# Kernel optimization log

Hardware: AMD Instinct MI355X
Metric: run time of the kernel (lower is better)

## Reference

```python
import jax, jax.numpy as jnp
import numpy as np

BUCKET_SIZE = 256
LOOK_BACKWARD = 1
LOOK_FORWARD = 0  # causal


def look_around(x, backward, forward, pad_value):
    # x: (b, n_buckets, w, ...) -> (b, n_buckets, w*(backward+forward+1), ...)
    n = x.shape[1]
    pads = [(0, 0)] * x.ndim
    pads[1] = (backward, forward)
    p = jnp.pad(x, pads, constant_values=pad_value)
    return jnp.concatenate([p[:, i:i + n] for i in range(backward + forward + 1)], axis=2)


def setup_inputs() -> dict:
    key = jax.random.key(0)
    kq, kk, kv = jax.random.split(key, 3)
    shape = (2, 16, 4096, 64)  # [batch, heads, seq, head_dim]
    q = jax.random.normal(kq, shape, dtype=jnp.float32)
    k = jax.random.normal(kk, shape, dtype=jnp.float32)
    v = jax.random.normal(kv, shape, dtype=jnp.float32)
    return {"q": q, "k": k, "v": v}


def reference(q, k, v):
    shape = q.shape
    t, e = shape[-2], shape[-1]
    merge = lambda x: x.reshape(-1, t, e)
    q, k, v = merge(q), merge(k), merge(v)
    b = q.shape[0]
    buckets = t // BUCKET_SIZE

    bucket_fn = lambda x: x.reshape(b, buckets, BUCKET_SIZE, e)
    bq, bk, bv = bucket_fn(q), bucket_fn(k), bucket_fn(v)

    bk = look_around(bk, LOOK_BACKWARD, LOOK_FORWARD, 0.0)
    bv = look_around(bv, LOOK_BACKWARD, LOOK_FORWARD, 0.0)

    ticker = jnp.arange(t, dtype=jnp.int32).reshape(1, buckets, BUCKET_SIZE)
    bq_t = ticker  # (1, buckets, w)
    bq_k = look_around(ticker, LOOK_BACKWARD, LOOK_FORWARD, -1)  # (1, buckets, w*(lb+lf+1))

    dots = jnp.einsum('bnie,bnje->bnij', bq, bk) * (e ** -0.5)
    mask_value = -jnp.finfo(dots.dtype).max

    causal_mask = bq_t[:, :, :, None] < bq_k[:, :, None, :]
    pad_mask = (bq_k == -1)[:, :, None, :]
    dots = jnp.where(causal_mask | pad_mask, mask_value, dots)

    attn = jax.nn.softmax(dots, axis=-1)
    out = jnp.einsum('bnij,bnje->bnie', attn, bv)
    return out.reshape(shape)
```

## Files before the change

kernel.cpp:

```cpp
#include <hip/hip_runtime.h>

typedef __bf16 bf16x8 __attribute__((ext_vector_type(8)));
typedef float f32x16 __attribute__((ext_vector_type(16)));
typedef int i32x2 __attribute__((ext_vector_type(2)));
typedef unsigned int u32;

static __device__ __forceinline__ u32 cvt_pk_bf16(float lo, float hi) {
    u32 r;
    asm("v_cvt_pk_bf16_f32 %0, %1, %2" : "=v"(r) : "v"(lo), "v"(hi));
    return r;
}

__global__ __launch_bounds__(256, 1)
void local_attn_kernel(const float* __restrict__ qg, const float* __restrict__ kg,
                       const float* __restrict__ vg, float* __restrict__ og)
{
    __shared__ __align__(16) __bf16 sK[2][64][64];
    __shared__ __align__(16) u32 sVp[2][64][32];

    const int bid = ((blockIdx.x & 7) << 7) | (blockIdx.x >> 3);
    const int bh = bid >> 5, bi = (bid >> 1) & 15, qh = bid & 1;
    const int tid = threadIdx.x, w = tid >> 6;
    const int lane = tid & 63, l31 = lane & 31, h = lane >> 5;

    const long long base = (long long)bh << 18;
    const float* qp = qg + base + ((long long)bi << 14);
    const float* kp = kg + base + (((long long)(bi - 1)) << 14);
    const float* vp = vg + base + (((long long)(bi - 1)) << 14);
    float*       op = og + base + ((long long)bi << 14);

    const int qb0 = qh * 128 + w * 32;

    bf16x8 qf[4];
    {
        const float QS = 0.18033688011112042f;
        const float* qrow = qp + (qb0 + l31) * 64 + 8 * h;
#pragma unroll
        for (int ks = 0; ks < 4; ++ks) {
            float4 f0 = *(const float4*)(qrow + ks * 16);
            float4 f1 = *(const float4*)(qrow + ks * 16 + 4);
            bf16x8 t;
            t[0] = (__bf16)(f0.x * QS); t[1] = (__bf16)(f0.y * QS);
            t[2] = (__bf16)(f0.z * QS); t[3] = (__bf16)(f0.w * QS);
            t[4] = (__bf16)(f1.x * QS); t[5] = (__bf16)(f1.y * QS);
            t[6] = (__bf16)(f1.z * QS); t[7] = (__bf16)(f1.w * QS);
            qf[ks] = t;
        }
    }

    f32x16 o0, o1;
#pragma unroll
    for (int i = 0; i < 16; ++i) { o0[i] = 0.f; o1[i] = 0.f; }
    float lsum = 0.f;

    const int skey = tid >> 3, stg = tid & 7;
    const int kslot = (stg ^ (skey & 7)) << 3;
    const int vkp = tid >> 4, vd0 = (tid & 15) * 4;
    const int vkq0 = vkp >> 2, vkq1 = vkq0 + 4, vj = vkp & 3;
    const int x0 = ((vd0 + 0) & 7) ^ (((vd0 + 0) >> 2) & 7);
    const int x1 = ((vd0 + 1) & 7) ^ (((vd0 + 1) >> 2) & 7);
    const int x2 = ((vd0 + 2) & 7) ^ (((vd0 + 2) >> 2) & 7);
    const int x3 = ((vd0 + 3) & 7) ^ (((vd0 + 3) >> 2) & 7);
    const float* kA = kp + skey * 64 + stg * 8;
    const float* vA = vp + (2 * vkp) * 64 + vd0;

    const int c0 = (bi == 0) ? 4 : 0;
    const int NCHB = 6 + 2 * qh;
    const int qpos = qb0 + l31;
    const int wlim = qb0 + 287;

    int cur = 0;
    float4 k0r, k1r, k2r, k3r, v0r, v1r, v2r, v3r;

#define STAGE_LOAD(c) do {                                   \
        const float* ks_ = kA + (c) * (64 * 64);             \
        k0r = *(const float4*)ks_;                           \
        k1r = *(const float4*)(ks_ + 4);                     \
        k2r = *(const float4*)(ks_ + 2048);                  \
        k3r = *(const float4*)(ks_ + 2052);                  \
        const float* vs_ = vA + (c) * (64 * 64);             \
        v0r = *(const float4*)vs_;                           \
        v1r = *(const float4*)(vs_ + 64);                    \
        v2r = *(const float4*)(vs_ + 2048);                  \
        v3r = *(const float4*)(vs_ + 2112);                  \
    } while (0)

#define STAGE_WRITE(buf) do {                                                     \
        union { u32 u[4]; bf16x8 b; } kva_, kvb_;                                 \
        kva_.u[0] = cvt_pk_bf16(k0r.x, k0r.y);                                    \
        kva_.u[1] = cvt_pk_bf16(k0r.z, k0r.w);                                    \
        kva_.u[2] = cvt_pk_bf16(k1r.x, k1r.y);                                    \
        kva_.u[3] = cvt_pk_bf16(k1r.z, k1r.w);                                    \
        *(bf16x8*)&sK[buf][skey][kslot] = kva_.b;                                 \
        kvb_.u[0] = cvt_pk_bf16(k2r.x, k2r.y);                                    \
        kvb_.u[1] = cvt_pk_bf16(k2r.z, k2r.w);                                    \
        kvb_.u[2] = cvt_pk_bf16(k3r.x, k3r.y);                                    \
        kvb_.u[3] = cvt_pk_bf16(k3r.z, k3r.w);                                    \
        *(bf16x8*)&sK[buf][skey + 32][kslot] = kvb_.b;                            \
        sVp[buf][vd0 + 0][((vkq0 ^ x0) << 2) + vj] = cvt_pk_bf16(v0r.x, v1r.x);   \
        sVp[buf][vd0 + 1][((vkq0 ^ x1) << 2) + vj] = cvt_pk_bf16(v0r.y, v1r.y);   \
        sVp[buf][vd0 + 2][((vkq0 ^ x2) << 2) + vj] = cvt_pk_bf16(v0r.z, v1r.z);   \
        sVp[buf][vd0 + 3][((vkq0 ^ x3) << 2) + vj] = cvt_pk_bf16(v0r.w, v1r.w);   \
        sVp[buf][vd0 + 0][((vkq1 ^ x0) << 2) + vj] = cvt_pk_bf16(v2r.x, v3r.x);   \
        sVp[buf][vd0 + 1][((vkq1 ^ x1) << 2) + vj] = cvt_pk_bf16(v2r.y, v3r.y);   \
        sVp[buf][vd0 + 2][((vkq1 ^ x2) << 2) + vj] = cvt_pk_bf16(v2r.z, v3r.z);   \
        sVp[buf][vd0 + 3][((vkq1 ^ x3) << 2) + vj] = cvt_pk_bf16(v2r.w, v3r.w);   \
    } while (0)

    STAGE_LOAD(c0);
    STAGE_WRITE(0);

    for (int c = c0; c < NCHB; ++c) {
        __syncthreads();
        const bool pf = (c + 1 < NCHB);
        if (pf) STAGE_LOAD(c + 1);

        const int kbase = c * 64;
#pragma unroll
        for (int kt = 0; kt < 2; ++kt) {
            const int kb0 = kbase + 32 * kt;
            if (kb0 > wlim) continue;

            const int key = kt * 32 + l31;
            const int ksw = key & 7;
            bf16x8 kfa[4];
#pragma unroll
            for (int ks = 0; ks < 4; ++ks)
                kfa[ks] = *(const bf16x8*)&sK[cur][key][((ks * 2 + h) ^ ksw) << 3];
            f32x16 s;
#pragma unroll
            for (int i2 = 0; i2 < 16; ++i2) s[i2] = 0.f;
#pragma unroll
            for (int ks = 0; ks < 4; ++ks)
                s = __builtin_amdgcn_mfma_f32_32x32x16_bf16(kfa[ks], qf[ks], s, 0, 0, 0);

            u32 wds[8];
            if (kb0 + 31 <= qb0 + 256) {
#pragma unroll
                for (int m = 0; m < 8; ++m) {
                    const float e0 = __builtin_amdgcn_exp2f(s[2 * m]);
                    const float e1 = __builtin_amdgcn_exp2f(s[2 * m + 1]);
                    lsum += e0 + e1;
                    wds[m] = cvt_pk_bf16(e0, e1);
                }
            } else {
                const int jb = kb0 + 4 * h;
#pragma unroll
                for (int m = 0; m < 8; ++m) {
                    const int r0 = 2 * m, r1 = 2 * m + 1;
                    const int j0 = jb + (r0 & 3) + 8 * (r0 >> 2);
                    const int j1 = jb + (r1 & 3) + 8 * (r1 >> 2);
                    float e0 = __builtin_amdgcn_exp2f(s[r0]);
                    float e1 = __builtin_amdgcn_exp2f(s[r1]);
                    e0 = (j0 > qpos + 256) ? 0.f : e0;
                    e1 = (j1 > qpos + 256) ? 0.f : e1;
                    lsum += e0 + e1;
                    wds[m] = cvt_pk_bf16(e0, e1);
                }
            }

#pragma unroll
            for (int kis = 0; kis < 2; ++kis) {
                i32x2 r02 = __builtin_amdgcn_permlane32_swap(
                    (int)wds[4 * kis + 0], (int)wds[4 * kis + 2], false, false);
                i32x2 r13 = __builtin_amdgcn_permlane32_swap(
                    (int)wds[4 * kis + 1], (int)wds[4 * kis + 3], false, false);
                union { u32 u[4]; bf16x8 b; } pu;
                pu.u[0] = (u32)r02.x; pu.u[1] = (u32)r13.x;
                pu.u[2] = (u32)r02.y; pu.u[3] = (u32)r13.y;

                const int G = (kt * 2 + kis) * 2 + h;
                const int sl = G ^ (l31 & 7) ^ ((l31 >> 2) & 7);
                bf16x8 vb0 = *(const bf16x8*)&sVp[cur][l31][sl << 2];
                bf16x8 vb1 = *(const bf16x8*)&sVp[cur][32 + l31][sl << 2];
                o0 = __builtin_amdgcn_mfma_f32_32x32x16_bf16(pu.b, vb0, o0, 0, 0, 0);
                o1 = __builtin_amdgcn_mfma_f32_32x32x16_bf16(pu.b, vb1, o1, 0, 0, 0);
            }
        }

        if (pf) STAGE_WRITE(cur ^ 1);
        cur ^= 1;
    }

    lsum += __shfl_xor(lsum, 32, 64);
    const float inv = 1.0f / lsum;
#pragma unroll
    for (int r = 0; r < 16; ++r) {
        const int qr = (r & 3) + 8 * (r >> 2) + 4 * h;
        const float iq = __shfl(inv, qr, 64);
        float* orow = op + (qb0 + qr) * 64;
        orow[l31]      = o0[r] * iq;
        orow[32 + l31] = o1[r] * iq;
    }
}

extern "C" void kernel_launch(void* const* d_in, const int* in_sizes, int n_in,
                              void* d_out, int out_size, void* d_ws, size_t ws_size,
                              hipStream_t stream) {
    const float* q = (const float*)d_in[0];
    const float* k = (const float*)d_in[1];
    const float* v = (const float*)d_in[2];
    float* out = (float*)d_out;
    local_attn_kernel<<<dim3(1024), dim3(256), 0, stream>>>(q, k, v, out);
}
```

Measured before the change: 42.07 us.

## Use one 512-thread block per bucket and load K directly from global

Merges the two query-half blocks into a single 512-thread block covering all 256 queries of a bucket, so the shared V staging is reused by eight waves instead of four and the grid halves. K is no longer staged in LDS; each wave reads its K rows from global memory and converts them to bf16 in registers right before the MFMA. This removes the K LDS traffic and the block-level duplication of V loads. In exchange, K is reloaded from global/L2 by every wave, and waves with short causal windows now sit through the same chunk loop and barriers as the longest one.

```diff
diff --git a/kernel.cpp b/kernel.cpp
--- a/kernel.cpp
+++ b/kernel.cpp
@@ -5,21 +5,22 @@
 typedef int i32x2 __attribute__((ext_vector_type(2)));
 typedef unsigned int u32;
 
+#define NCH 8
+
 static __device__ __forceinline__ u32 cvt_pk_bf16(float lo, float hi) {
     u32 r;
     asm("v_cvt_pk_bf16_f32 %0, %1, %2" : "=v"(r) : "v"(lo), "v"(hi));
     return r;
 }
 
-__global__ __launch_bounds__(256, 1)
+__global__ __launch_bounds__(512, 2)
 void local_attn_kernel(const float* __restrict__ qg, const float* __restrict__ kg,
                        const float* __restrict__ vg, float* __restrict__ og)
 {
-    __shared__ __align__(16) __bf16 sK[2][64][64];
     __shared__ __align__(16) u32 sVp[2][64][32];
 
-    const int bid = ((blockIdx.x & 7) << 7) | (blockIdx.x >> 3);
-    const int bh = bid >> 5, bi = (bid >> 1) & 15, qh = bid & 1;
+    const int bid = ((blockIdx.x & 7) << 6) | (blockIdx.x >> 3);
+    const int bh = bid >> 4, bi = bid & 15;
     const int tid = threadIdx.x, w = tid >> 6;
     const int lane = tid & 63, l31 = lane & 31, h = lane >> 5;
 
@@ -29,12 +30,10 @@
     const float* vp = vg + base + (((long long)(bi - 1)) << 14);
     float*       op = og + base + ((long long)bi << 14);
 
-    const int qb0 = qh * 128 + w * 32;
-
     bf16x8 qf[4];
     {
         const float QS = 0.18033688011112042f;
-        const float* qrow = qp + (qb0 + l31) * 64 + 8 * h;
+        const float* qrow = qp + (w * 32 + l31) * 64 + 8 * h;
 #pragma unroll
         for (int ks = 0; ks < 4; ++ks) {
             float4 f0 = *(const float4*)(qrow + ks * 16);
@@ -53,66 +52,40 @@
     for (int i = 0; i < 16; ++i) { o0[i] = 0.f; o1[i] = 0.f; }
     float lsum = 0.f;
 
-    const int skey = tid >> 3, stg = tid & 7;
-    const int kslot = (stg ^ (skey & 7)) << 3;
     const int vkp = tid >> 4, vd0 = (tid & 15) * 4;
-    const int vkq0 = vkp >> 2, vkq1 = vkq0 + 4, vj = vkp & 3;
+    const int vkq = vkp >> 2, vj = vkp & 3;
     const int x0 = ((vd0 + 0) & 7) ^ (((vd0 + 0) >> 2) & 7);
     const int x1 = ((vd0 + 1) & 7) ^ (((vd0 + 1) >> 2) & 7);
     const int x2 = ((vd0 + 2) & 7) ^ (((vd0 + 2) >> 2) & 7);
     const int x3 = ((vd0 + 3) & 7) ^ (((vd0 + 3) >> 2) & 7);
-    const float* kA = kp + skey * 64 + stg * 8;
     const float* vA = vp + (2 * vkp) * 64 + vd0;
 
     const int c0 = (bi == 0) ? 4 : 0;
-    const int NCHB = 6 + 2 * qh;
-    const int qpos = qb0 + l31;
-    const int wlim = qb0 + 287;
+    const int qpos = w * 32 + l31;
+    const int wlim = 32 * w + 287;
 
     int cur = 0;
-    float4 k0r, k1r, k2r, k3r, v0r, v1r, v2r, v3r;
+    float4 v0r, v1r;
 
 #define STAGE_LOAD(c) do {                                   \
-        const float* ks_ = kA + (c) * (64 * 64);             \
-        k0r = *(const float4*)ks_;                           \
-        k1r = *(const float4*)(ks_ + 4);                     \
-        k2r = *(const float4*)(ks_ + 2048);                  \
-        k3r = *(const float4*)(ks_ + 2052);                  \
         const float* vs_ = vA + (c) * (64 * 64);             \
         v0r = *(const float4*)vs_;                           \
         v1r = *(const float4*)(vs_ + 64);                    \
-        v2r = *(const float4*)(vs_ + 2048);                  \
-        v3r = *(const float4*)(vs_ + 2112);                  \
     } while (0)
 
 #define STAGE_WRITE(buf) do {                                                     \
-        union { u32 u[4]; bf16x8 b; } kva_, kvb_;                                 \
-        kva_.u[0] = cvt_pk_bf16(k0r.x, k0r.y);                                    \
-        kva_.u[1] = cvt_pk_bf16(k0r.z, k0r.w);                                    \
-        kva_.u[2] = cvt_pk_bf16(k1r.x, k1r.y);                                    \
-        kva_.u[3] = cvt_pk_bf16(k1r.z, k1r.w);                                    \
-        *(bf16x8*)&sK[buf][skey][kslot] = kva_.b;                                 \
-        kvb_.u[0] = cvt_pk_bf16(k2r.x, k2r.y);                                    \
-        kvb_.u[1] = cvt_pk_bf16(k2r.z, k2r.w);                                    \
-        kvb_.u[2] = cvt_pk_bf16(k3r.x, k3r.y);                                    \
-        kvb_.u[3] = cvt_pk_bf16(k3r.z, k3r.w);                                    \
-        *(bf16x8*)&sK[buf][skey + 32][kslot] = kvb_.b;                            \
-        sVp[buf][vd0 + 0][((vkq0 ^ x0) << 2) + vj] = cvt_pk_bf16(v0r.x, v1r.x);   \
-        sVp[buf][vd0 + 1][((vkq0 ^ x1) << 2) + vj] = cvt_pk_bf16(v0r.y, v1r.y);   \
-        sVp[buf][vd0 + 2][((vkq0 ^ x2) << 2) + vj] = cvt_pk_bf16(v0r.z, v1r.z);   \
-        sVp[buf][vd0 + 3][((vkq0 ^ x3) << 2) + vj] = cvt_pk_bf16(v0r.w, v1r.w);   \
-        sVp[buf][vd0 + 0][((vkq1 ^ x0) << 2) + vj] = cvt_pk_bf16(v2r.x, v3r.x);   \
-        sVp[buf][vd0 + 1][((vkq1 ^ x1) << 2) + vj] = cvt_pk_bf16(v2r.y, v3r.y);   \
-        sVp[buf][vd0 + 2][((vkq1 ^ x2) << 2) + vj] = cvt_pk_bf16(v2r.z, v3r.z);   \
-        sVp[buf][vd0 + 3][((vkq1 ^ x3) << 2) + vj] = cvt_pk_bf16(v2r.w, v3r.w);   \
+        sVp[buf][vd0 + 0][((vkq ^ x0) << 2) + vj] = cvt_pk_bf16(v0r.x, v1r.x);    \
+        sVp[buf][vd0 + 1][((vkq ^ x1) << 2) + vj] = cvt_pk_bf16(v0r.y, v1r.y);    \
+        sVp[buf][vd0 + 2][((vkq ^ x2) << 2) + vj] = cvt_pk_bf16(v0r.z, v1r.z);    \
+        sVp[buf][vd0 + 3][((vkq ^ x3) << 2) + vj] = cvt_pk_bf16(v0r.w, v1r.w);    \
     } while (0)
 
     STAGE_LOAD(c0);
     STAGE_WRITE(0);
 
-    for (int c = c0; c < NCHB; ++c) {
+    for (int c = c0; c < NCH; ++c) {
         __syncthreads();
-        const bool pf = (c + 1 < NCHB);
+        const bool pf = (c + 1 < NCH);
         if (pf) STAGE_LOAD(c + 1);
 
         const int kbase = c * 64;
@@ -121,12 +94,20 @@
             const int kb0 = kbase + 32 * kt;
             if (kb0 > wlim) continue;
 
-            const int key = kt * 32 + l31;
-            const int ksw = key & 7;
+            const float* krow = kp + (long long)(kb0 + l31) * 64 + 8 * h;
             bf16x8 kfa[4];
 #pragma unroll
-            for (int ks = 0; ks < 4; ++ks)
-                kfa[ks] = *(const bf16x8*)&sK[cur][key][((ks * 2 + h) ^ ksw) << 3];
+            for (int ks = 0; ks < 4; ++ks) {
+                const float4 a = *(const float4*)(krow + ks * 16);
+                const float4 b = *(const float4*)(krow + ks * 16 + 4);
+                union { u32 u[4]; bf16x8 v; } kk;
+                kk.u[0] = cvt_pk_bf16(a.x, a.y);
+                kk.u[1] = cvt_pk_bf16(a.z, a.w);
+                kk.u[2] = cvt_pk_bf16(b.x, b.y);
+                kk.u[3] = cvt_pk_bf16(b.z, b.w);
+                kfa[ks] = kk.v;
+            }
+
             f32x16 s;
 #pragma unroll
             for (int i2 = 0; i2 < 16; ++i2) s[i2] = 0.f;
@@ -135,7 +116,7 @@
                 s = __builtin_amdgcn_mfma_f32_32x32x16_bf16(kfa[ks], qf[ks], s, 0, 0, 0);
 
             u32 wds[8];
-            if (kb0 + 31 <= qb0 + 256) {
+            if (kb0 + 31 <= 32 * w + 256) {
 #pragma unroll
                 for (int m = 0; m < 8; ++m) {
                     const float e0 = __builtin_amdgcn_exp2f(s[2 * m]);
@@ -188,7 +169,7 @@
     for (int r = 0; r < 16; ++r) {
         const int qr = (r & 3) + 8 * (r >> 2) + 4 * h;
         const float iq = __shfl(inv, qr, 64);
-        float* orow = op + (qb0 + qr) * 64;
+        float* orow = op + (w * 32 + qr) * 64;
         orow[l31]      = o0[r] * iq;
         orow[32 + l31] = o1[r] * iq;
     }
@@ -201,5 +182,5 @@
     const float* k = (const float*)d_in[1];
     const float* v = (const float*)d_in[2];
     float* out = (float*)d_out;
-    local_attn_kernel<<<dim3(1024), dim3(256), 0, stream>>>(q, k, v, out);
+    local_attn_kernel<<<dim3(512), dim3(512), 0, stream>>>(q, k, v, out);
 }
```

After: 66.86 us. 1.59x slower.
